# Kernel tuning notes

Hardware: AMD Instinct MI355X
Metric: run time of the kernel (lower is better)

## Reference

```python
import jax, jax.numpy as jnp
import numpy as np

B, T, H, NH = 4, 2048, 2048, 16
HD = H // NH
SCALE = HD ** -0.5

def setup_inputs() -> dict:
    key = jax.random.key(0)
    ks = jax.random.split(key, 9)
    s = H ** -0.5
    return {
        "x": jax.random.normal(ks[0], (B, T, H), jnp.float32),
        "q_w": jax.random.normal(ks[1], (H, H), jnp.float32) * s,
        "q_b": jnp.zeros((H,), jnp.float32),
        "k_w": jax.random.normal(ks[2], (H, H), jnp.float32) * s,
        "k_b": jnp.zeros((H,), jnp.float32),
        "v_w": jax.random.normal(ks[3], (H, H), jnp.float32) * s,
        "v_b": jnp.zeros((H,), jnp.float32),
        "o_w": jax.random.normal(ks[4], (H, H), jnp.float32) * s,
        "o_b": jnp.zeros((H,), jnp.float32),
    }

def reference(x, q_w, q_b, k_w, k_b, v_w, v_b, o_w, o_b):
    Bd, Td, Hd = x.shape
    # projections (torch Linear: y = x @ W^T + b)
    q = (x @ q_w.T + q_b).reshape(Bd, Td, NH, HD).transpose(0, 2, 1, 3)  # [B,nh,T,hd]
    k = (x @ k_w.T + k_b).reshape(Bd, Td, NH, HD).transpose(0, 2, 1, 3)
    v = (x @ v_w.T + v_b).reshape(Bd, Td, NH, HD).transpose(0, 2, 1, 3)
    scores = jnp.einsum('bhqd,bhkd->bhqk', q, k) * SCALE  # [B,nh,T,T]
    causal = jnp.tril(jnp.ones((Td, Td), dtype=bool))
    scores = jnp.where(causal, scores, -jnp.inf)
    probs = jax.nn.softmax(scores, axis=-1)
    ctx = jnp.einsum('bhqk,bhkd->bhqd', probs, v)  # [B,nh,T,hd]
    ctx = ctx.transpose(0, 2, 1, 3).reshape(Bd, Td, Hd)
    return ctx @ o_w.T + o_b
```

## Files before the change

### kernel.cpp

```cpp
#include <hip/hip_runtime.h>
#include <stdint.h>

#define B_SZ 4
#define T_SEQ 2048
#define H_DIM 2048
#define NH_ 16
#define HD_ 128
#define MTOK (B_SZ * T_SEQ)

typedef __attribute__((ext_vector_type(8))) short bf16x8;
typedef __attribute__((ext_vector_type(4))) float f32x4;
typedef __attribute__((ext_vector_type(4))) unsigned short u16x4;

__device__ __forceinline__ unsigned short f2b(float f) {
  union { float f; uint32_t u; } x; x.f = f;
  uint32_t r = x.u + 0x7FFFu + ((x.u >> 16) & 1u);
  return (unsigned short)(r >> 16);
}

__device__ __forceinline__ void gload16(const void* g, void* l) {
  __builtin_amdgcn_global_load_lds((const __attribute__((address_space(1))) void*)g,
                                   (__attribute__((address_space(3))) void*)l, 16, 0, 0);
}

__global__ void cvt_bf16_k(const float* __restrict__ in, unsigned short* __restrict__ out, int n4) {
  for (int i = blockIdx.x * blockDim.x + threadIdx.x; i < n4; i += gridDim.x * blockDim.x) {
    float4 v = ((const float4*)in)[i];
    u16x4 o;
    o[0] = f2b(v.x); o[1] = f2b(v.y); o[2] = f2b(v.z); o[3] = f2b(v.w);
    ((u16x4*)out)[i] = o;
  }
}

template <int MODE>
__global__ __launch_bounds__(512, 2) void gemm256_k(const unsigned short* __restrict__ A,
                                                    const unsigned short* __restrict__ W,
                                                    const float* __restrict__ bias,
                                                    void* __restrict__ outp) {
  constexpr int K = H_DIM;
  constexpr int NT = K / 64;
  __shared__ __align__(16) unsigned short Al[2][256 * 64];
  __shared__ __align__(16) unsigned short Bl[2][256 * 64];

  const int tid = threadIdx.x;
  const int w = tid >> 6, l = tid & 63;
  const int g = l >> 4, ln = l & 15;
  const int wr = w >> 2, wc = w & 3;

  const int bid = blockIdx.x + gridDim.x * blockIdx.y;
  const int fid = ((bid & 7) << 5) | (bid >> 3);
  const int col0 = (fid & 7) * 256;
  const int row0 = (fid >> 3) * 256;

  const char* Ag = (const char*)A;
  const char* Wg = (const char*)W;

  const int srow = l >> 3;
  const int sbyte = ((l & 7) * 16) ^ (srow << 4);

#define ST_A(t2, b2, c)                                                                 \
  gload16(Ag + (((size_t)(row0 + (c) * 8 + srow)) * K + (t2) * 64) * 2 + sbyte,         \
          (char*)&Al[b2][0] + (c) * 1024)
#define ST_B(t2, b2, c)                                                                 \
  gload16(Wg + (((size_t)(col0 + (c) * 8 + srow)) * K + (t2) * 64) * 2 + sbyte,         \
          (char*)&Bl[b2][0] + (c) * 1024)
#define STAGE_A0(t2, b2) do { ST_A(t2, b2, w);  ST_A(t2, b2, 16 + w); } while (0)
#define STAGE_A1(t2, b2) do { ST_A(t2, b2, 8 + w); ST_A(t2, b2, 24 + w); } while (0)
#define STAGE_B0(t2, b2) do { int c_ = (w >> 2) * 8 + (w & 3); ST_B(t2, b2, c_); ST_B(t2, b2, 16 + c_); } while (0)
#define STAGE_B1(t2, b2) do { int c_ = (w >> 2) * 8 + 4 + (w & 3); ST_B(t2, b2, c_); ST_B(t2, b2, 16 + c_); } while (0)

  f32x4 acc[8][4] = {};
  bf16x8 aF[4][2];
  bf16x8 bF[2][2][2];

#define READ_A(mh)                                                                      \
  _Pragma("unroll") for (int mf = 0; mf < 4; ++mf)                                      \
  _Pragma("unroll") for (int ks = 0; ks < 2; ++ks) {                                    \
    int row_ = wr * 128 + (mh) * 64 + mf * 16 + ln;                                     \
    aF[mf][ks] = *(const bf16x8*)((const char*)Ab + row_ * 128 +                        \
                                  ((ks * 64 + g * 16) ^ ((ln & 7) << 4)));              \
  }
#define READ_B(nh)                                                                      \
  _Pragma("unroll") for (int nf = 0; nf < 2; ++nf)                                      \
  _Pragma("unroll") for (int ks = 0; ks < 2; ++ks) {                                    \
    int row_ = wc * 64 + (nh) * 32 + nf * 16 + ln;                                      \
    bF[nh][nf][ks] = *(const bf16x8*)((const char*)Bb + row_ * 128 +                    \
                                      ((ks * 64 + g * 16) ^ ((ln & 7) << 4)));          \
  }
#define MFMA_PHASE(mh, nh)                                                              \
  do {                                                                                  \
    __builtin_amdgcn_s_setprio(1);                                                      \
    _Pragma("unroll") for (int mf = 0; mf < 4; ++mf)                                    \
    _Pragma("unroll") for (int nf = 0; nf < 2; ++nf)                                    \
    _Pragma("unroll") for (int ks = 0; ks < 2; ++ks)                                    \
      acc[(mh) * 4 + mf][(nh) * 2 + nf] = __builtin_amdgcn_mfma_f32_16x16x32_bf16(      \
          aF[mf][ks], bF[nh][nf][ks], acc[(mh) * 4 + mf][(nh) * 2 + nf], 0, 0, 0);      \
    __builtin_amdgcn_s_setprio(0);                                                      \
  } while (0)
#define BARRIER() asm volatile("s_barrier" ::: "memory")

  STAGE_A0(0, 0); STAGE_B0(0, 0); STAGE_B1(0, 0); STAGE_A1(0, 0);
  STAGE_A0(1, 1); STAGE_B0(1, 1); STAGE_B1(1, 1); STAGE_A1(1, 1);
  asm volatile("s_waitcnt vmcnt(8)" ::: "memory");
  BARRIER();

#pragma unroll 1
  for (int t = 0; t < NT; ++t) {
    const int buf = t & 1;
    const unsigned short* Ab = &Al[buf][0];
    const unsigned short* Bb = &Bl[buf][0];
    READ_A(0); READ_B(0);
    if (t >= 1 && t + 1 < NT) STAGE_A1(t + 1, (t + 1) & 1);
    BARRIER();
    MFMA_PHASE(0, 0);
    BARRIER();
    READ_B(1);
    if (t + 2 < NT) STAGE_A0(t + 2, buf);
    BARRIER();
    MFMA_PHASE(0, 1);
    BARRIER();
    READ_A(1);
    if (t + 2 < NT) STAGE_B0(t + 2, buf);
    BARRIER();
    MFMA_PHASE(1, 0);
    BARRIER();
    if (t + 2 < NT) {
      STAGE_B1(t + 2, buf);
      asm volatile("s_waitcnt vmcnt(6)" ::: "memory");
    } else {
      asm volatile("s_waitcnt vmcnt(0)" ::: "memory");
    }
    BARRIER();
    MFMA_PHASE(1, 1);
    BARRIER();
  }

#pragma unroll
  for (int mi = 0; mi < 8; ++mi) {
#pragma unroll
    for (int ni = 0; ni < 4; ++ni) {
      int n = col0 + wc * 64 + ni * 16 + ln;
      float bv = bias[n];
      if constexpr (MODE == 2) {
        float* out = (float*)outp;
#pragma unroll
        for (int r = 0; r < 4; ++r) {
          int m = row0 + wr * 128 + mi * 16 + 4 * g + r;
          out[(size_t)m * H_DIM + n] = acc[mi][ni][r] + bv;
        }
      } else if constexpr (MODE == 0) {
        unsigned short* out = (unsigned short*)outp;
        int h = n >> 7, d = n & 127;
#pragma unroll
        for (int r = 0; r < 4; ++r) {
          int m = row0 + wr * 128 + mi * 16 + 4 * g + r;
          int b = m >> 11, tt = m & 2047;
          out[(((size_t)(b * NH_ + h)) * T_SEQ + tt) * HD_ + d] = f2b(acc[mi][ni][r] + bv);
        }
      } else {
        unsigned short* out = (unsigned short*)outp;
        int h = n >> 7, d = n & 127;
        int m0 = row0 + wr * 128 + mi * 16 + 4 * g;
        int b = m0 >> 11, t0 = m0 & 2047;
        u16x4 pk;
#pragma unroll
        for (int r = 0; r < 4; ++r) pk[r] = f2b(acc[mi][ni][r] + bv);
        *(u16x4*)&out[(((size_t)(b * NH_ + h)) * HD_ + d) * T_SEQ + t0] = pk;
      }
    }
  }
#undef ST_A
#undef ST_B
#undef STAGE_A0
#undef STAGE_A1
#undef STAGE_B0
#undef STAGE_B1
#undef READ_A
#undef READ_B
#undef MFMA_PHASE
#undef BARRIER
}

__global__ __launch_bounds__(512) void attn256_k(const unsigned short* __restrict__ Q,
                                                 const unsigned short* __restrict__ Kg,
                                                 const unsigned short* __restrict__ Vt,
                                                 unsigned short* __restrict__ ctx) {
  __shared__ __align__(16) unsigned short Kl[2][64 * 128];
  __shared__ __align__(16) unsigned short Vl[2][128 * 64];
  __shared__ __align__(16) unsigned short Pl[8][32 * 80];

  const int tid = threadIdx.x;
  const int w = tid >> 6, l = tid & 63;
  const int g = l >> 4, ln = l & 15;

  const int flat = ((blockIdx.x & 7) << 5) | (blockIdx.x >> 3);
  const int qi = flat & 3;
  const int bh = flat >> 2;

  const float cscale = 0.08838834764831845f * 1.4426950408889634f;

  const char* kbase = (const char*)(Kg + (size_t)bh * T_SEQ * HD_);
  const char* vbase = (const char*)(Vt + (size_t)bh * HD_ * T_SEQ);
  unsigned short* Pw = &Pl[w][0];
  const int b = bh >> 4, h = bh & 15;

#define STAGE_KV(bufi, ktile) do {                                                    \
    int kv0_ = (ktile) * 64;                                                          \
    _Pragma("unroll")                                                                 \
    for (int i_ = 0; i_ < 2; ++i_) {                                                  \
      int c_ = w * 2 + i_;                                                            \
      int kvr_ = c_ * 4 + g;                                                          \
      gload16(kbase + ((size_t)(kv0_ + kvr_) * HD_) * 2 + ((ln * 16) ^ ((kvr_ & 7) << 4)), \
              (char*)&Kl[bufi][0] + c_ * 1024);                                       \
      int d_ = c_ * 8 + (l >> 3);                                                     \
      gload16(vbase + ((size_t)d_ * T_SEQ + kv0_) * 2 + (((l & 7) * 16) ^ ((d_ & 7) << 4)), \
              (char*)&Vl[bufi][0] + c_ * 1024);                                       \
    } } while (0)

#pragma unroll 1
  for (int half = 0; half < 2; ++half) {
    const int qt = half ? qi : (7 - qi);
    const int q0 = qt << 8;
    const int qw = q0 + w * 32;

    bf16x8 bq[2][4];
#pragma unroll
    for (int f = 0; f < 2; ++f)
#pragma unroll
      for (int kk = 0; kk < 4; ++kk)
        bq[f][kk] = *(const bf16x8*)(Q + ((size_t)bh * T_SEQ + qw + f * 16 + ln) * HD_ + kk * 32 + g * 8);

    f32x4 acc[2][8] = {};
    float mrun[2] = {-INFINITY, -INFINITY};
    float lrun[2] = {0.f, 0.f};

    const int nt = (qt + 1) * 4;

    STAGE_KV(0, 0);
    __syncthreads();
    int cur = 0;

#pragma unroll 1
    for (int kt = 0; kt < nt; ++kt) {
      if (kt + 1 < nt) STAGE_KV(cur ^ 1, kt + 1);
      const int kv0 = kt * 64;
      if (kv0 <= qw + 31) {
        const char* kl = (const char*)&Kl[cur][0];
        const char* vl = (const char*)&Vl[cur][0];

        f32x4 st[2][4] = {};
#pragma unroll
        for (int kk = 0; kk < 4; ++kk) {
          bf16x8 ak[4];
#pragma unroll
          for (int mf = 0; mf < 4; ++mf)
            ak[mf] = *(const bf16x8*)(kl + (mf * 16 + ln) * 256 + ((kk * 64 + g * 16) ^ ((ln & 7) << 4)));
#pragma unroll
          for (int mf = 0; mf < 4; ++mf) {
            st[0][mf] = __builtin_amdgcn_mfma_f32_16x16x32_bf16(ak[mf], bq[0][kk], st[0][mf], 0, 0, 0);
            st[1][mf] = __builtin_amdgcn_mfma_f32_16x16x32_bf16(ak[mf], bq[1][kk], st[1][mf], 0, 0, 0);
          }
        }

        if (kv0 + 63 > qw) {
#pragma unroll
          for (int f = 0; f < 2; ++f)
#pragma unroll
            for (int mf = 0; mf < 4; ++mf)
#pragma unroll
              for (int r = 0; r < 4; ++r)
                if (kv0 + mf * 16 + g * 4 + r > qw + f * 16 + ln) st[f][mf][r] = -INFINITY;
        }

#pragma unroll
        for (int f = 0; f < 2; ++f) {
          float pmax = -INFINITY;
#pragma unroll
          for (int mf = 0; mf < 4; ++mf)
#pragma unroll
            for (int r = 0; r < 4; ++r) pmax = fmaxf(pmax, st[f][mf][r]);
          pmax = fmaxf(pmax, __shfl_xor(pmax, 16));
          pmax = fmaxf(pmax, __shfl_xor(pmax, 32));
          float mnew = fmaxf(mrun[f], pmax * cscale);
          float fac = __builtin_amdgcn_exp2f(mrun[f] - mnew);

          float psum = 0.f;
#pragma unroll
          for (int mf = 0; mf < 4; ++mf) {
            u16x4 pk;
#pragma unroll
            for (int r = 0; r < 4; ++r) {
              float p = __builtin_amdgcn_exp2f(st[f][mf][r] * cscale - mnew);
              psum += p;
              pk[r] = f2b(p);
            }
            *(u16x4*)&Pw[(f * 16 + ln) * 80 + mf * 16 + g * 4] = pk;
          }
          psum += __shfl_xor(psum, 16);
          psum += __shfl_xor(psum, 32);
          lrun[f] = lrun[f] * fac + psum;
          mrun[f] = mnew;

          float fr[4];
#pragma unroll
          for (int r = 0; r < 4; ++r) fr[r] = __shfl(fac, g * 4 + r);
#pragma unroll
          for (int nf = 0; nf < 8; ++nf) {
            acc[f][nf][0] *= fr[0]; acc[f][nf][1] *= fr[1];
            acc[f][nf][2] *= fr[2]; acc[f][nf][3] *= fr[3];
          }

          bf16x8 ap[2];
#pragma unroll
          for (int ks = 0; ks < 2; ++ks)
            ap[ks] = *(const bf16x8*)((const char*)Pw + (f * 16 + ln) * 160 + ks * 64 + g * 16);
#pragma unroll
          for (int nf = 0; nf < 8; ++nf) {
            int d = nf * 16 + ln;
#pragma unroll
            for (int ks = 0; ks < 2; ++ks) {
              bf16x8 bv = *(const bf16x8*)(vl + d * 128 + ((ks * 64 + g * 16) ^ ((ln & 7) << 4)));
              acc[f][nf] = __builtin_amdgcn_mfma_f32_16x16x32_bf16(ap[ks], bv, acc[f][nf], 0, 0, 0);
            }
          }
        }
      }
      __syncthreads();
      cur ^= 1;
    }

#pragma unroll
    for (int f = 0; f < 2; ++f) {
      float inv[4];
#pragma unroll
      for (int r = 0; r < 4; ++r) inv[r] = 1.f / __shfl(lrun[f], g * 4 + r);
#pragma unroll
      for (int nf = 0; nf < 8; ++nf) {
#pragma unroll
        for (int r = 0; r < 4; ++r) {
          int qrow = qw + f * 16 + g * 4 + r;
          ctx[((size_t)(b * T_SEQ + qrow)) * H_DIM + h * HD_ + nf * 16 + ln] =
              f2b(acc[f][nf][r] * inv[r]);
        }
      }
    }
  }
#undef STAGE_KV
}

extern "C" void kernel_launch(void* const* d_in, const int* in_sizes, int n_in,
                              void* d_out, int out_size, void* d_ws, size_t ws_size,
                              hipStream_t stream) {
  (void)in_sizes; (void)n_in; (void)out_size; (void)ws_size;
  const float* x  = (const float*)d_in[0];
  const float* qw = (const float*)d_in[1];
  const float* qb = (const float*)d_in[2];
  const float* kw = (const float*)d_in[3];
  const float* kb = (const float*)d_in[4];
  const float* vw = (const float*)d_in[5];
  const float* vb = (const float*)d_in[6];
  const float* ow = (const float*)d_in[7];
  const float* ob = (const float*)d_in[8];

  char* ws = (char*)d_ws;
  unsigned short* xb  = (unsigned short*)(ws);
  unsigned short* qwb = (unsigned short*)(ws + 33554432);
  unsigned short* kwb = (unsigned short*)(ws + 41943040);
  unsigned short* vwb = (unsigned short*)(ws + 50331648);
  unsigned short* owb = (unsigned short*)(ws + 58720256);
  unsigned short* Qb  = (unsigned short*)(ws + 67108864);
  unsigned short* Kb  = (unsigned short*)(ws + 100663296);
  unsigned short* Vtb = (unsigned short*)(ws + 134217728);
  unsigned short* ctxb = xb;

  dim3 blk(256);
  cvt_bf16_k<<<2048, blk, 0, stream>>>(x,  xb,  (MTOK * H_DIM) / 4);
  cvt_bf16_k<<<1024, blk, 0, stream>>>(qw, qwb, (H_DIM * H_DIM) / 4);
  cvt_bf16_k<<<1024, blk, 0, stream>>>(kw, kwb, (H_DIM * H_DIM) / 4);
  cvt_bf16_k<<<1024, blk, 0, stream>>>(vw, vwb, (H_DIM * H_DIM) / 4);
  cvt_bf16_k<<<1024, blk, 0, stream>>>(ow, owb, (H_DIM * H_DIM) / 4);

  dim3 ggrid(H_DIM / 256, MTOK / 256);
  dim3 gblk(512);
  gemm256_k<0><<<ggrid, gblk, 0, stream>>>(xb, qwb, qb, Qb);
  gemm256_k<0><<<ggrid, gblk, 0, stream>>>(xb, kwb, kb, Kb);
  gemm256_k<1><<<ggrid, gblk, 0, stream>>>(xb, vwb, vb, Vtb);

  attn256_k<<<dim3(256), dim3(512), 0, stream>>>(Qb, Kb, Vtb, ctxb);

  gemm256_k<2><<<ggrid, gblk, 0, stream>>>(ctxb, owb, ob, (float*)d_out);
}
```

Measured before the change: 430.8 us.

## Keep attention P in registers via lane shuffles, lazy rescale, setprio, shared V reads

Drops the per-wave LDS staging buffer for the softmax probabilities and instead packs P to bf16 with v_cvt_pk_bf16_f32, then rearranges it across lanes with shuffles into the MFMA A-operand layout. The online-softmax rescale of the accumulators is now done only when the running max grows by more than a threshold, which skips most rescale multiplies. The PV matmul is merged across both query fragments so each V tile read from LDS feeds two MFMAs. MFMA sections are wrapped in s_setprio, and launch bounds now request two blocks per CU. The costs are extra shuffle instructions, higher register pressure under the occupancy hint, and a small numerical risk from the lazy max threshold.

After: 408.5 us. 5.2% less time.

```diff
diff --git a/kernel.cpp b/kernel.cpp
--- a/kernel.cpp
+++ b/kernel.cpp
@@ -181,13 +181,12 @@
 #undef BARRIER
 }
 
-__global__ __launch_bounds__(512) void attn256_k(const unsigned short* __restrict__ Q,
-                                                 const unsigned short* __restrict__ Kg,
-                                                 const unsigned short* __restrict__ Vt,
-                                                 unsigned short* __restrict__ ctx) {
+__global__ __launch_bounds__(512, 2) void attn256_k(const unsigned short* __restrict__ Q,
+                                                    const unsigned short* __restrict__ Kg,
+                                                    const unsigned short* __restrict__ Vt,
+                                                    unsigned short* __restrict__ ctx) {
   __shared__ __align__(16) unsigned short Kl[2][64 * 128];
   __shared__ __align__(16) unsigned short Vl[2][128 * 64];
-  __shared__ __align__(16) unsigned short Pl[8][32 * 80];
 
   const int tid = threadIdx.x;
   const int w = tid >> 6, l = tid & 63;
@@ -201,7 +200,6 @@
 
   const char* kbase = (const char*)(Kg + (size_t)bh * T_SEQ * HD_);
   const char* vbase = (const char*)(Vt + (size_t)bh * HD_ * T_SEQ);
-  unsigned short* Pw = &Pl[w][0];
   const int b = bh >> 4, h = bh & 15;
 
 #define STAGE_KV(bufi, ktile) do {                                                    \
@@ -249,6 +247,7 @@
         const char* vl = (const char*)&Vl[cur][0];
 
         f32x4 st[2][4] = {};
+        __builtin_amdgcn_s_setprio(1);
 #pragma unroll
         for (int kk = 0; kk < 4; ++kk) {
           bf16x8 ak[4];
@@ -261,6 +260,7 @@
             st[1][mf] = __builtin_amdgcn_mfma_f32_16x16x32_bf16(ak[mf], bq[1][kk], st[1][mf], 0, 0, 0);
           }
         }
+        __builtin_amdgcn_s_setprio(0);
 
         if (kv0 + 63 > qw) {
 #pragma unroll
@@ -272,6 +272,7 @@
                 if (kv0 + mf * 16 + g * 4 + r > qw + f * 16 + ln) st[f][mf][r] = -INFINITY;
         }
 
+        bf16x8 ap[2][2];
 #pragma unroll
         for (int f = 0; f < 2; ++f) {
           float pmax = -INFINITY;
@@ -281,49 +282,67 @@
             for (int r = 0; r < 4; ++r) pmax = fmaxf(pmax, st[f][mf][r]);
           pmax = fmaxf(pmax, __shfl_xor(pmax, 16));
           pmax = fmaxf(pmax, __shfl_xor(pmax, 32));
-          float mnew = fmaxf(mrun[f], pmax * cscale);
-          float fac = __builtin_amdgcn_exp2f(mrun[f] - mnew);
-
+          float tmax = pmax * cscale;
+          float msub = mrun[f];
+          if (__any(tmax > mrun[f] + 8.f)) {
+            msub = fmaxf(mrun[f], tmax);
+            float fac = __builtin_amdgcn_exp2f(mrun[f] - msub);
+            mrun[f] = msub;
+            lrun[f] *= fac;
+            float fr[4];
+#pragma unroll
+            for (int r = 0; r < 4; ++r) fr[r] = __shfl(fac, g * 4 + r);
+#pragma unroll
+            for (int nf = 0; nf < 8; ++nf) {
+              acc[f][nf][0] *= fr[0]; acc[f][nf][1] *= fr[1];
+              acc[f][nf][2] *= fr[2]; acc[f][nf][3] *= fr[3];
+            }
+          }
+          uint32_t Aq[4][2];
           float psum = 0.f;
 #pragma unroll
           for (int mf = 0; mf < 4; ++mf) {
-            u16x4 pk;
-#pragma unroll
-            for (int r = 0; r < 4; ++r) {
-              float p = __builtin_amdgcn_exp2f(st[f][mf][r] * cscale - mnew);
-              psum += p;
-              pk[r] = f2b(p);
-            }
-            *(u16x4*)&Pw[(f * 16 + ln) * 80 + mf * 16 + g * 4] = pk;
+            float p0 = __builtin_amdgcn_exp2f(st[f][mf][0] * cscale - msub);
+            float p1 = __builtin_amdgcn_exp2f(st[f][mf][1] * cscale - msub);
+            float p2 = __builtin_amdgcn_exp2f(st[f][mf][2] * cscale - msub);
+            float p3 = __builtin_amdgcn_exp2f(st[f][mf][3] * cscale - msub);
+            psum += (p0 + p1) + (p2 + p3);
+            asm("v_cvt_pk_bf16_f32 %0, %1, %2" : "=v"(Aq[mf][0]) : "v"(p0), "v"(p1));
+            asm("v_cvt_pk_bf16_f32 %0, %1, %2" : "=v"(Aq[mf][1]) : "v"(p2), "v"(p3));
           }
           psum += __shfl_xor(psum, 16);
           psum += __shfl_xor(psum, 32);
-          lrun[f] = lrun[f] * fac + psum;
-          mrun[f] = mnew;
-
-          float fr[4];
-#pragma unroll
-          for (int r = 0; r < 4; ++r) fr[r] = __shfl(fac, g * 4 + r);
-#pragma unroll
-          for (int nf = 0; nf < 8; ++nf) {
-            acc[f][nf][0] *= fr[0]; acc[f][nf][1] *= fr[1];
-            acc[f][nf][2] *= fr[2]; acc[f][nf][3] *= fr[3];
+          lrun[f] += psum;
+
+#pragma unroll
+          for (int ks = 0; ks < 2; ++ks) {
+            union { uint32_t u[4]; bf16x8 v; } t;
+#pragma unroll
+            for (int dw = 0; dw < 2; ++dw) {
+              uint32_t u0 = (g < 2) ? Aq[2 * ks][dw] : Aq[2 * ks + 1][dw];
+              uint32_t w0 = (g < 2) ? Aq[2 * ks + 1][dw] : Aq[2 * ks][dw];
+              uint32_t u16v = __shfl_xor(u0, 16);
+              uint32_t w32v = __shfl_xor(w0, 32);
+              uint32_t w48v = __shfl_xor(w0, 48);
+              t.u[dw]     = (g == 0) ? u0   : (g == 1) ? w48v : (g == 2) ? w32v : u16v;
+              t.u[2 + dw] = (g == 0) ? u16v : (g == 1) ? w32v : (g == 2) ? w48v : u0;
+            }
+            ap[f][ks] = t.v;
           }
-
-          bf16x8 ap[2];
-#pragma unroll
-          for (int ks = 0; ks < 2; ++ks)
-            ap[ks] = *(const bf16x8*)((const char*)Pw + (f * 16 + ln) * 160 + ks * 64 + g * 16);
-#pragma unroll
-          for (int nf = 0; nf < 8; ++nf) {
-            int d = nf * 16 + ln;
-#pragma unroll
-            for (int ks = 0; ks < 2; ++ks) {
-              bf16x8 bv = *(const bf16x8*)(vl + d * 128 + ((ks * 64 + g * 16) ^ ((ln & 7) << 4)));
-              acc[f][nf] = __builtin_amdgcn_mfma_f32_16x16x32_bf16(ap[ks], bv, acc[f][nf], 0, 0, 0);
-            }
+        }
+
+        __builtin_amdgcn_s_setprio(1);
+#pragma unroll
+        for (int nf = 0; nf < 8; ++nf) {
+          int d = nf * 16 + ln;
+#pragma unroll
+          for (int ks = 0; ks < 2; ++ks) {
+            bf16x8 bv = *(const bf16x8*)(vl + d * 128 + ((ks * 64 + g * 16) ^ ((ln & 7) << 4)));
+            acc[0][nf] = __builtin_amdgcn_mfma_f32_16x16x32_bf16(ap[0][ks], bv, acc[0][nf], 0, 0, 0);
+            acc[1][nf] = __builtin_amdgcn_mfma_f32_16x16x32_bf16(ap[1][ks], bv, acc[1][nf], 0, 0, 0);
           }
         }
+        __builtin_amdgcn_s_setprio(0);
       }
       __syncthreads();
       cur ^= 1;
```
